# Kernel tuning notes

Hardware: AMD Instinct MI355X
Metric: run time of the kernel (lower is better)

## Reference

```python
import jax, jax.numpy as jnp
import numpy as np

EPS = 1e-5
DIM, QK, PDIM, SR = 256, 64, 128, 2
B, H, W = 16, 64, 64
SCALE = QK ** (-0.5)


def _conv(x, w, stride, pad, groups=1):
    return jax.lax.conv_general_dilated(
        x, w, (stride, stride), [(pad, pad), (pad, pad)], feature_group_count=groups)


def _bn(x, g, b, m, v):
    # inference-mode BatchNorm2d with running stats
    s = (g / jnp.sqrt(v + EPS))[None, :, None, None]
    return (x - m[None, :, None, None]) * s + b[None, :, None, None]


def _gn1(x, g, b):
    # GroupNorm(1, C): normalize over (C,H,W) per sample
    mu = x.mean(axis=(1, 2, 3), keepdims=True)
    var = x.var(axis=(1, 2, 3), keepdims=True)
    xh = (x - mu) / jnp.sqrt(var + EPS)
    return xh * g[None, :, None, None] + b[None, :, None, None]


def setup_inputs() -> dict:
    key = jax.random.key(0)
    ks = jax.random.split(key, 6)
    inp = {
        'x': jax.random.normal(ks[0], (B, DIM, H, W), jnp.float32),
        'gn_g': jnp.ones((DIM,), jnp.float32),
        'gn_b': jnp.zeros((DIM,), jnp.float32),
        'w_in': jax.random.normal(ks[1], (2 * QK + DIM, DIM, 3, 3), jnp.float32) * 0.05,
        'bn_in_g': jnp.ones((2 * QK + DIM,), jnp.float32),
        'bn_in_b': jnp.zeros((2 * QK + DIM,), jnp.float32),
        'bn_in_m': jnp.zeros((2 * QK + DIM,), jnp.float32),
        'bn_in_v': jnp.ones((2 * QK + DIM,), jnp.float32),
        'w_k': jax.random.normal(ks[2], (QK, 1, SR, SR), jnp.float32) * 0.05,
        'bn_k_g': jnp.ones((QK,), jnp.float32),
        'bn_k_b': jnp.zeros((QK,), jnp.float32),
        'bn_k_m': jnp.zeros((QK,), jnp.float32),
        'bn_k_v': jnp.ones((QK,), jnp.float32),
        'w_v': jax.random.normal(ks[3], (PDIM, 1, SR, SR), jnp.float32) * 0.05,
        'bn_v_g': jnp.ones((PDIM,), jnp.float32),
        'bn_v_b': jnp.zeros((PDIM,), jnp.float32),
        'bn_v_m': jnp.zeros((PDIM,), jnp.float32),
        'bn_v_v': jnp.ones((PDIM,), jnp.float32),
        'w_out': jax.random.normal(ks[4], (DIM, DIM, 1, 1), jnp.float32) * 0.05,
        'bn_out_g': jnp.ones((DIM,), jnp.float32),
        'bn_out_b': jnp.zeros((DIM,), jnp.float32),
        'bn_out_m': jnp.zeros((DIM,), jnp.float32),
        'bn_out_v': jnp.ones((DIM,), jnp.float32),
    }
    return inp


def reference(x, gn_g, gn_b, w_in, bn_in_g, bn_in_b, bn_in_m, bn_in_v,
              w_k, bn_k_g, bn_k_b, bn_k_m, bn_k_v,
              w_v, bn_v_g, bn_v_b, bn_v_m, bn_v_v,
              w_out, bn_out_g, bn_out_b, bn_out_m, bn_out_v):
    x = _gn1(x, gn_g, gn_b)
    y = _bn(_conv(x, w_in, 1, 1), bn_in_g, bn_in_b, bn_in_m, bn_in_v)
    q = y[:, :QK]
    k = y[:, QK:2 * QK]
    v = y[:, 2 * QK:2 * QK + PDIM]
    u = y[:, 2 * QK + PDIM:]
    # depthwise sr-stride convs reduce k/v spatially
    k = _bn(_conv(k, w_k, SR, 0, groups=QK), bn_k_g, bn_k_b, bn_k_m, bn_k_v)
    v = _bn(_conv(v, w_v, SR, 0, groups=PDIM), bn_v_g, bn_v_b, bn_v_m, bn_v_v)
    b, _, h, w = u.shape
    qf = q.reshape(b, QK, -1)      # [B, QK, N]
    kf = k.reshape(b, QK, -1)      # [B, QK, M]
    vf = v.reshape(b, PDIM, -1)    # [B, PDIM, M]
    attn = jnp.einsum('bcn,bcm->bnm', qf, kf) * SCALE
    attn = jax.nn.softmax(attn, axis=-1)
    o = jnp.einsum('bcm,bnm->bcn', vf, attn).reshape(b, PDIM, h, w)
    cat = jnp.concatenate([o, u], axis=1)
    out = _bn(_conv(jax.nn.relu(cat), w_out, 1, 0), bn_out_g, bn_out_b, bn_out_m, bn_out_v)
    return out
```

## Files before the change

### kernel.cpp

```cpp
#include <hip/hip_runtime.h>
#include <stdint.h>

#define EPSV 1e-5f

typedef __attribute__((ext_vector_type(8))) short short8;
typedef __attribute__((ext_vector_type(4))) float f32x4;
typedef __bf16 bf16x8 __attribute__((ext_vector_type(8)));

__device__ __forceinline__ unsigned short f2bf(float f) {
  union { float f; unsigned int u; } v; v.f = f;
  unsigned int r = (v.u + 0x7FFFu + ((v.u >> 16) & 1u)) >> 16;
  return (unsigned short)r;
}
__device__ __forceinline__ float bf2f(unsigned short h) {
  union { unsigned int u; float f; } v; v.u = ((unsigned int)h) << 16;
  return v.f;
}

__device__ __forceinline__ f32x4 mfma16(bf16x8 a, bf16x8 b, f32x4 c) {
  return __builtin_amdgcn_mfma_f32_16x16x32_bf16(a, b, c, 0, 0, 0);
}

#define GLOAD16(g, l)                                                          \
  __builtin_amdgcn_global_load_lds(                                            \
      (const __attribute__((address_space(1))) void*)(g),                      \
      (__attribute__((address_space(3))) void*)(l), 16, 0, 0)

__global__ __launch_bounds__(256) void k_gn_stats(const float* __restrict__ x,
                                                  float* __restrict__ stats) {
  int b = blockIdx.x >> 6, chunk = blockIdx.x & 63;
  const float4* xp = (const float4*)(x + ((size_t)b << 20) + (size_t)chunk * 16384);
  int t = threadIdx.x;
  float s = 0.f, q = 0.f;
#pragma unroll
  for (int i = 0; i < 16; ++i) {
    float4 v = xp[i * 256 + t];
    s += v.x + v.y + v.z + v.w;
    q += v.x * v.x + v.y * v.y + v.z * v.z + v.w * v.w;
  }
#pragma unroll
  for (int m = 1; m <= 32; m <<= 1) { s += __shfl_xor(s, m); q += __shfl_xor(q, m); }
  __shared__ float ls[8];
  int w = t >> 6, l = t & 63;
  if (l == 0) { ls[w * 2] = s; ls[w * 2 + 1] = q; }
  __syncthreads();
  if (t == 0) {
    float S = ls[0] + ls[2] + ls[4] + ls[6];
    float Q = ls[1] + ls[3] + ls[5] + ls[7];
    atomicAdd(&stats[b * 2], S);
    atomicAdd(&stats[b * 2 + 1], Q);
  }
}

__global__ __launch_bounds__(256) void k_gn_norm(const float* __restrict__ x,
                                                 const float* __restrict__ stats,
                                                 const float* __restrict__ g,
                                                 const float* __restrict__ bb,
                                                 unsigned short* __restrict__ xnp) {
  __shared__ float tile[64][65];
  int pt = blockIdx.x;
  int ct = blockIdx.y;
  int b = blockIdx.z;
  int t = threadIdx.x, tr = t >> 6, tc = t & 63;
  const float* xb = x + ((size_t)b << 20) + (size_t)(ct * 64) * 4096 + pt * 64;
#pragma unroll
  for (int i = 0; i < 16; ++i) {
    int r = i * 4 + tr;
    tile[r][tc] = xb[(size_t)r * 4096 + tc];
  }
  __syncthreads();
  float mu = stats[b * 2] * (1.f / 1048576.f);
  float var = stats[b * 2 + 1] * (1.f / 1048576.f) - mu * mu;
  float istd = rsqrtf(var + EPSV);
  float gg = g[ct * 64 + tc] * istd;
  float bv = bb[ct * 64 + tc];
  unsigned short* out = xnp + (((size_t)b * 66 + (pt + 1)) * 66 + 1) * 256 + ct * 64 + tc;
#pragma unroll
  for (int i = 0; i < 16; ++i) {
    int pcol = i * 4 + tr;
    float v = (tile[tc][pcol] - mu) * gg + bv;
    out[(size_t)pcol * 256] = f2bf(v);
  }
}

__global__ __launch_bounds__(256) void k_prep_wt(const float* __restrict__ w_in,
                                                 const float* __restrict__ bg,
                                                 const float* __restrict__ bv,
                                                 unsigned short* __restrict__ wt) {
  int idx = blockIdx.x * 256 + threadIdx.x;
  if (idx >= 9 * 384 * 256) return;
  int tap = idx / 98304;
  int rem = idx - tap * 98304;
  int co = rem >> 8, ci = rem & 255;
  float s = bg[co] * rsqrtf(bv[co] + EPSV);
  wt[idx] = f2bf(w_in[(size_t)(co * 256 + ci) * 9 + tap] * s);
}

__global__ __launch_bounds__(256) void k_prep_misc(
    const float* w_out, const float* og, const float* ob, const float* om, const float* ov,
    const float* big, const float* bib, const float* bim, const float* biv,
    const float* w_k, const float* kg, const float* kb, const float* km, const float* kvv,
    const float* w_v, const float* vg, const float* vb, const float* vm, const float* vvv,
    unsigned short* wo2, float* bias_in, float* bias_out,
    float* wkf, float* bias_k, float* wvf, float* bias_v) {
  int idx = blockIdx.x * 256 + threadIdx.x;
  if (idx < 65536) {
    int co = idx >> 8;
    float s = og[co] * rsqrtf(ov[co] + EPSV);
    wo2[idx] = f2bf(w_out[idx] * s);
    return;
  }
  idx -= 65536;
  if (idx < 384) {
    float s = big[idx] * rsqrtf(biv[idx] + EPSV);
    bias_in[idx] = bib[idx] - bim[idx] * s;
    return;
  }
  idx -= 384;
  if (idx < 256) {
    float s = og[idx] * rsqrtf(ov[idx] + EPSV);
    bias_out[idx] = ob[idx] - om[idx] * s;
    return;
  }
  idx -= 256;
  if (idx < 64) {
    float s = kg[idx] * rsqrtf(kvv[idx] + EPSV);
#pragma unroll
    for (int tp = 0; tp < 4; ++tp) wkf[idx * 4 + tp] = w_k[idx * 4 + tp] * s;
    bias_k[idx] = kb[idx] - km[idx] * s;
    return;
  }
  idx -= 64;
  if (idx < 128) {
    float s = vg[idx] * rsqrtf(vvv[idx] + EPSV);
#pragma unroll
    for (int tp = 0; tp < 4; ++tp) wvf[idx * 4 + tp] = w_v[idx * 4 + tp] * s;
    bias_v[idx] = vb[idx] - vm[idx] * s;
    return;
  }
}

__global__ __launch_bounds__(256) void k_conv3(const unsigned short* __restrict__ xnp,
                                               const unsigned short* __restrict__ wt,
                                               const float* __restrict__ bias_in,
                                               unsigned short* __restrict__ y) {
  int pt = blockIdx.x, cot = blockIdx.y, b = blockIdx.z;
  int p0 = pt * 128, co0 = cot * 128;
  __shared__ alignas(16) unsigned short As[128 * 64];
  __shared__ alignas(16) unsigned short Bs[128 * 64];
  int t = threadIdx.x, w = t >> 6, l = t & 63;
  int rr = t >> 3, c8 = (t & 7) * 8;
  int lg = l >> 4, lr = l & 15;

  int baseA[4];
#pragma unroll
  for (int i = 0; i < 4; ++i) {
    int p = p0 + i * 32 + rr;
    int yy = p >> 6, xx = p & 63;
    baseA[i] = ((b * 66 + yy) * 66 + xx) * 256 + c8;
  }
  int baseB = (co0 + rr) * 256 + c8;

  f32x4 acc[4][4];
#pragma unroll
  for (int i = 0; i < 4; ++i)
#pragma unroll
    for (int j = 0; j < 4; ++j) acc[i][j] = f32x4{0.f, 0.f, 0.f, 0.f};

  int wr = (w >> 1) * 64, wc = (w & 1) * 64;

  for (int tap = 0; tap < 9; ++tap) {
    int aoff = ((tap / 3) * 66 + (tap % 3)) * 256;
#pragma unroll 1
    for (int kc = 0; kc < 4; ++kc) {
      int ci0 = kc * 64;
      __syncthreads();
#pragma unroll
      for (int i = 0; i < 4; ++i) {
        GLOAD16(xnp + baseA[i] + aoff + ci0, &As[(i * 32 + w * 8) * 64]);
        GLOAD16(wt + baseB + tap * 98304 + i * 8192 + ci0, &Bs[(i * 32 + w * 8) * 64]);
      }
      __syncthreads();
      bf16x8 af[4][2], bf[4][2];
#pragma unroll
      for (int mt = 0; mt < 4; ++mt)
#pragma unroll
        for (int k2 = 0; k2 < 2; ++k2) {
          af[mt][k2] = *(const bf16x8*)&As[(wr + mt * 16 + lr) * 64 + k2 * 32 + lg * 8];
          bf[mt][k2] = *(const bf16x8*)&Bs[(wc + mt * 16 + lr) * 64 + k2 * 32 + lg * 8];
        }
#pragma unroll
      for (int mt = 0; mt < 4; ++mt)
#pragma unroll
        for (int nt = 0; nt < 4; ++nt) {
          acc[mt][nt] = mfma16(af[mt][0], bf[nt][0], acc[mt][nt]);
          acc[mt][nt] = mfma16(af[mt][1], bf[nt][1], acc[mt][nt]);
        }
    }
  }
  float bias[4];
  int coBase = co0 + wc;
#pragma unroll
  for (int nt = 0; nt < 4; ++nt) bias[nt] = bias_in[coBase + nt * 16 + lr];
#pragma unroll
  for (int mt = 0; mt < 4; ++mt) {
    int p = p0 + wr + mt * 16 + lg * 4;
#pragma unroll
    for (int r = 0; r < 4; ++r) {
      size_t rowoff = ((size_t)(b * 4096 + p + r)) * 384;
#pragma unroll
      for (int nt = 0; nt < 4; ++nt) {
        int co = coBase + nt * 16 + lr;
        float v = acc[mt][nt][r] + bias[nt];
        if (co >= 256) v = fmaxf(v, 0.f);
        y[rowoff + co] = f2bf(v);
      }
    }
  }
}

__global__ __launch_bounds__(256) void k_kv(const unsigned short* __restrict__ y,
                                            const float* __restrict__ wkf, const float* __restrict__ bias_k,
                                            const float* __restrict__ wvf, const float* __restrict__ bias_v,
                                            unsigned short* __restrict__ kk, unsigned short* __restrict__ vv) {
  int idx = blockIdx.x * 256 + threadIdx.x;
  if (idx < 16 * 1024 * 64) {
    int c = idx & 63, m = (idx >> 6) & 1023, b = idx >> 16;
    int my = m >> 5, mx = m & 31;
    float acc = bias_k[c];
#pragma unroll
    for (int tp = 0; tp < 4; ++tp) {
      int dy = tp >> 1, dx = tp & 1;
      int p = (2 * my + dy) * 64 + 2 * mx + dx;
      acc += bf2f(y[((size_t)(b * 4096 + p)) * 384 + 64 + c]) * wkf[c * 4 + tp];
    }
    kk[idx] = f2bf(acc);
  } else {
    int i2 = idx - 16 * 1024 * 64;
    if (i2 >= 16 * 128 * 1024) return;
    int m = i2 & 1023, cv = (i2 >> 10) & 127, b = i2 >> 17;
    int my = m >> 5, mx = m & 31;
    float acc = bias_v[cv];
#pragma unroll
    for (int tp = 0; tp < 4; ++tp) {
      int dy = tp >> 1, dx = tp & 1;
      int p = (2 * my + dy) * 64 + 2 * mx + dx;
      acc += bf2f(y[((size_t)(b * 4096 + p)) * 384 + 128 + cv]) * wvf[cv * 4 + tp];
    }
    vv[i2] = f2bf(acc);
  }
}

__global__ __launch_bounds__(256) void k_attn(unsigned short* __restrict__ y,
                                              const unsigned short* __restrict__ kk,
                                              const unsigned short* __restrict__ vvb) {
  int blk = blockIdx.x;
  int b = blk >> 5, ntile = blk & 31;
  int t = threadIdx.x, w = t >> 6, l = t & 63;
  int nq0 = ntile * 128 + w * 32;
  int lg = l >> 4, lr = l & 15;
  __shared__ alignas(16) unsigned short P[4][2][16][64];
  const float SC = 0.125f * 1.44269504f;

  bf16x8 qf[2][2];
#pragma unroll
  for (int qt = 0; qt < 2; ++qt)
#pragma unroll
    for (int c = 0; c < 2; ++c)
      qf[qt][c] = *(const bf16x8*)&y[((size_t)(b * 4096 + nq0 + qt * 16 + lr)) * 384 + c * 32 + lg * 8];

  f32x4 oa[2][8];
#pragma unroll
  for (int qt = 0; qt < 2; ++qt)
#pragma unroll
    for (int tt = 0; tt < 8; ++tt) oa[qt][tt] = f32x4{0.f, 0.f, 0.f, 0.f};
  float mi[2][4], li[2][4];
#pragma unroll
  for (int qt = 0; qt < 2; ++qt)
#pragma unroll
    for (int r = 0; r < 4; ++r) { mi[qt][r] = -1e30f; li[qt][r] = 0.f; }

  for (int m0 = 0; m0 < 1024; m0 += 64) {
    bf16x8 kf[4][2];
#pragma unroll
    for (int mt = 0; mt < 4; ++mt)
#pragma unroll
      for (int c = 0; c < 2; ++c)
        kf[mt][c] = *(const bf16x8*)&kk[((size_t)(b * 1024 + m0 + mt * 16 + lr)) * 64 + c * 32 + lg * 8];

#pragma unroll
    for (int qt = 0; qt < 2; ++qt) {
      f32x4 s[4];
#pragma unroll
      for (int mt = 0; mt < 4; ++mt) {
        f32x4 z = f32x4{0.f, 0.f, 0.f, 0.f};
        z = mfma16(qf[qt][0], kf[mt][0], z);
        z = mfma16(qf[qt][1], kf[mt][1], z);
        s[mt] = z;
      }
#pragma unroll
      for (int mt = 0; mt < 4; ++mt)
#pragma unroll
        for (int r = 0; r < 4; ++r) s[mt][r] *= SC;
      float rm[4];
#pragma unroll
      for (int r = 0; r < 4; ++r)
        rm[r] = fmaxf(fmaxf(s[0][r], s[1][r]), fmaxf(s[2][r], s[3][r]));
#pragma unroll
      for (int msk = 1; msk <= 8; msk <<= 1)
#pragma unroll
        for (int r = 0; r < 4; ++r) rm[r] = fmaxf(rm[r], __shfl_xor(rm[r], msk));
      float corr[4], rs[4];
#pragma unroll
      for (int r = 0; r < 4; ++r) {
        float nm = fmaxf(mi[qt][r], rm[r]);
        corr[r] = exp2f(mi[qt][r] - nm);
        mi[qt][r] = nm;
#pragma unroll
        for (int mt = 0; mt < 4; ++mt) s[mt][r] = exp2f(s[mt][r] - nm);
        rs[r] = s[0][r] + s[1][r] + s[2][r] + s[3][r];
      }
#pragma unroll
      for (int msk = 1; msk <= 8; msk <<= 1)
#pragma unroll
        for (int r = 0; r < 4; ++r) rs[r] += __shfl_xor(rs[r], msk);
#pragma unroll
      for (int r = 0; r < 4; ++r) li[qt][r] = li[qt][r] * corr[r] + rs[r];
#pragma unroll
      for (int tt = 0; tt < 8; ++tt)
#pragma unroll
        for (int r = 0; r < 4; ++r) oa[qt][tt][r] *= corr[r];
#pragma unroll
      for (int mt = 0; mt < 4; ++mt)
#pragma unroll
        for (int r = 0; r < 4; ++r)
          P[w][qt][lg * 4 + r][mt * 16 + lr] = f2bf(s[mt][r]);
    }
    __builtin_amdgcn_wave_barrier();
    bf16x8 pf[2][2];
#pragma unroll
    for (int qt = 0; qt < 2; ++qt)
#pragma unroll
      for (int mc = 0; mc < 2; ++mc)
        pf[qt][mc] = *(const bf16x8*)&P[w][qt][lr][mc * 32 + lg * 8];
#pragma unroll
    for (int tt = 0; tt < 8; ++tt) {
      bf16x8 vf0 = *(const bf16x8*)&vvb[((size_t)(b * 128 + tt * 16 + lr)) * 1024 + m0 + lg * 8];
      bf16x8 vf1 = *(const bf16x8*)&vvb[((size_t)(b * 128 + tt * 16 + lr)) * 1024 + m0 + 32 + lg * 8];
#pragma unroll
      for (int qt = 0; qt < 2; ++qt) {
        oa[qt][tt] = mfma16(pf[qt][0], vf0, oa[qt][tt]);
        oa[qt][tt] = mfma16(pf[qt][1], vf1, oa[qt][tt]);
      }
    }
  }
#pragma unroll
  for (int qt = 0; qt < 2; ++qt)
#pragma unroll
    for (int r = 0; r < 4; ++r) {
      float inv = 1.f / li[qt][r];
      int p = nq0 + qt * 16 + lg * 4 + r;
#pragma unroll
      for (int tt = 0; tt < 8; ++tt) {
        float v = oa[qt][tt][r] * inv;
        v = fmaxf(v, 0.f);
        y[((size_t)(b * 4096 + p)) * 384 + 128 + tt * 16 + lr] = f2bf(v);
      }
    }
}

__global__ __launch_bounds__(256) void k_conv1(const unsigned short* __restrict__ y,
                                               const unsigned short* __restrict__ wo2,
                                               const float* __restrict__ bias_out,
                                               float* __restrict__ out) {
  int ptile = blockIdx.x, cot = blockIdx.y, b = blockIdx.z;
  int p0 = ptile * 128, co0 = cot * 128;
  __shared__ alignas(16) unsigned short As[128 * 64];
  __shared__ alignas(16) unsigned short Bs[128 * 64];
  int t = threadIdx.x, w = t >> 6, l = t & 63;
  int rr = t >> 3, c8 = (t & 7) * 8;
  int lg = l >> 4, lr = l & 15;
  int baseA = (co0 + rr) * 256 + c8;
  size_t baseB = ((size_t)(b * 4096 + p0 + rr)) * 384 + 128 + c8;
  f32x4 acc[4][4];
#pragma unroll
  for (int i = 0; i < 4; ++i)
#pragma unroll
    for (int j = 0; j < 4; ++j) acc[i][j] = f32x4{0.f, 0.f, 0.f, 0.f};
  int wr = (w >> 1) * 64, wc = (w & 1) * 64;
#pragma unroll 1
  for (int kc = 0; kc < 4; ++kc) {
    int ci0 = kc * 64;
    __syncthreads();
#pragma unroll
    for (int i = 0; i < 4; ++i) {
      GLOAD16(wo2 + baseA + i * 8192 + ci0, &As[(i * 32 + w * 8) * 64]);
      GLOAD16(y + baseB + (size_t)i * 32 * 384 + ci0, &Bs[(i * 32 + w * 8) * 64]);
    }
    __syncthreads();
    bf16x8 af[4][2], bf[4][2];
#pragma unroll
    for (int mt = 0; mt < 4; ++mt)
#pragma unroll
      for (int k2 = 0; k2 < 2; ++k2) {
        af[mt][k2] = *(const bf16x8*)&As[(wr + mt * 16 + lr) * 64 + k2 * 32 + lg * 8];
        bf[mt][k2] = *(const bf16x8*)&Bs[(wc + mt * 16 + lr) * 64 + k2 * 32 + lg * 8];
      }
#pragma unroll
    for (int mt = 0; mt < 4; ++mt)
#pragma unroll
      for (int nt = 0; nt < 4; ++nt) {
        acc[mt][nt] = mfma16(af[mt][0], bf[nt][0], acc[mt][nt]);
        acc[mt][nt] = mfma16(af[mt][1], bf[nt][1], acc[mt][nt]);
      }
  }
#pragma unroll
  for (int mt = 0; mt < 4; ++mt)
#pragma unroll
    for (int r = 0; r < 4; ++r) {
      int co = co0 + wr + mt * 16 + lg * 4 + r;
      float bv = bias_out[co];
      size_t obase = ((size_t)(b * 256 + co)) << 12;
#pragma unroll
      for (int nt = 0; nt < 4; ++nt) {
        int p = p0 + wc + nt * 16 + lr;
        out[obase + p] = acc[mt][nt][r] + bv;
      }
    }
}

static constexpr size_t pad256(size_t x) { return (x + 255) & ~(size_t)255; }

extern "C" void kernel_launch(void* const* d_in, const int* in_sizes, int n_in,
                              void* d_out, int out_size, void* d_ws, size_t ws_size,
                              hipStream_t stream) {
  const float* x      = (const float*)d_in[0];
  const float* gn_g   = (const float*)d_in[1];
  const float* gn_b   = (const float*)d_in[2];
  const float* w_in   = (const float*)d_in[3];
  const float* bin_g  = (const float*)d_in[4];
  const float* bin_b  = (const float*)d_in[5];
  const float* bin_m  = (const float*)d_in[6];
  const float* bin_v  = (const float*)d_in[7];
  const float* w_k    = (const float*)d_in[8];
  const float* bk_g   = (const float*)d_in[9];
  const float* bk_b   = (const float*)d_in[10];
  const float* bk_m   = (const float*)d_in[11];
  const float* bk_v   = (const float*)d_in[12];
  const float* w_v    = (const float*)d_in[13];
  const float* bv_g   = (const float*)d_in[14];
  const float* bv_b   = (const float*)d_in[15];
  const float* bv_m   = (const float*)d_in[16];
  const float* bv_v   = (const float*)d_in[17];
  const float* w_out  = (const float*)d_in[18];
  const float* bo_g   = (const float*)d_in[19];
  const float* bo_b   = (const float*)d_in[20];
  const float* bo_m   = (const float*)d_in[21];
  const float* bo_v   = (const float*)d_in[22];
  float* out = (float*)d_out;

  char* ws = (char*)d_ws;
  size_t off = 0;
  float*          stats   = (float*)(ws + off);          off += pad256(128);
  unsigned short* wt      = (unsigned short*)(ws + off); off += pad256((size_t)9 * 384 * 256 * 2);
  float*          bias_in = (float*)(ws + off);          off += pad256(384 * 4);
  unsigned short* wo2     = (unsigned short*)(ws + off); off += pad256(256 * 256 * 2);
  float*          bias_out= (float*)(ws + off);          off += pad256(256 * 4);
  float*          wkf     = (float*)(ws + off);          off += pad256(64 * 4 * 4);
  float*          bias_k  = (float*)(ws + off);          off += pad256(64 * 4);
  float*          wvf     = (float*)(ws + off);          off += pad256(128 * 4 * 4);
  float*          bias_v  = (float*)(ws + off);          off += pad256(128 * 4);
  unsigned short* xnp     = (unsigned short*)(ws + off); off += pad256((size_t)16 * 66 * 66 * 256 * 2);
  unsigned short* y       = (unsigned short*)(ws + off); off += pad256((size_t)16 * 4096 * 384 * 2);
  unsigned short* kk      = (unsigned short*)(ws + off); off += pad256((size_t)16 * 1024 * 64 * 2);
  unsigned short* vv      = (unsigned short*)(ws + off); off += pad256((size_t)16 * 128 * 1024 * 2);
  (void)ws_size; (void)out_size; (void)n_in; (void)in_sizes;

  hipMemsetAsync(stats, 0, 256, stream);
  hipMemsetAsync(xnp, 0, (size_t)16 * 66 * 66 * 256 * 2, stream);

  k_gn_stats<<<1024, 256, 0, stream>>>(x, stats);
  k_prep_wt<<<3456, 256, 0, stream>>>(w_in, bin_g, bin_v, wt);
  k_prep_misc<<<260, 256, 0, stream>>>(w_out, bo_g, bo_b, bo_m, bo_v,
                                       bin_g, bin_b, bin_m, bin_v,
                                       w_k, bk_g, bk_b, bk_m, bk_v,
                                       w_v, bv_g, bv_b, bv_m, bv_v,
                                       wo2, bias_in, bias_out, wkf, bias_k, wvf, bias_v);
  k_gn_norm<<<dim3(64, 4, 16), 256, 0, stream>>>(x, stats, gn_g, gn_b, xnp);
  k_conv3<<<dim3(32, 3, 16), 256, 0, stream>>>(xnp, wt, bias_in, y);
  k_kv<<<12288, 256, 0, stream>>>(y, wkf, bias_k, wvf, bias_v, kk, vv);
  k_attn<<<512, 256, 0, stream>>>(y, kk, vv);
  k_conv1<<<dim3(32, 2, 16), 256, 0, stream>>>(y, wo2, bias_out, out);
}
```

Before: 492.9 us.

## Stage k/v reduction through LDS; lazy softmax rescale and MFMA row sums

```diff
diff --git a/kernel.cpp b/kernel.cpp
--- a/kernel.cpp
+++ b/kernel.cpp
@@ -223,31 +223,65 @@
                                             const float* __restrict__ wkf, const float* __restrict__ bias_k,
                                             const float* __restrict__ wvf, const float* __restrict__ bias_v,
                                             unsigned short* __restrict__ kk, unsigned short* __restrict__ vv) {
-  int idx = blockIdx.x * 256 + threadIdx.x;
-  if (idx < 16 * 1024 * 64) {
-    int c = idx & 63, m = (idx >> 6) & 1023, b = idx >> 16;
-    int my = m >> 5, mx = m & 31;
-    float acc = bias_k[c];
-#pragma unroll
-    for (int tp = 0; tp < 4; ++tp) {
-      int dy = tp >> 1, dx = tp & 1;
-      int p = (2 * my + dy) * 64 + 2 * mx + dx;
-      acc += bf2f(y[((size_t)(b * 4096 + p)) * 384 + 64 + c]) * wkf[c * 4 + tp];
-    }
-    kk[idx] = f2bf(acc);
-  } else {
-    int i2 = idx - 16 * 1024 * 64;
-    if (i2 >= 16 * 128 * 1024) return;
-    int m = i2 & 1023, cv = (i2 >> 10) & 127, b = i2 >> 17;
-    int my = m >> 5, mx = m & 31;
-    float acc = bias_v[cv];
-#pragma unroll
-    for (int tp = 0; tp < 4; ++tp) {
-      int dy = tp >> 1, dx = tp & 1;
-      int p = (2 * my + dy) * 64 + 2 * mx + dx;
-      acc += bf2f(y[((size_t)(b * 4096 + p)) * 384 + 128 + cv]) * wvf[cv * 4 + tp];
-    }
-    vv[i2] = f2bf(acc);
+  constexpr int LDW = 200;
+  __shared__ unsigned short ty[128 * LDW];
+  __shared__ unsigned short vt[128 * 33];
+  int b = blockIdx.x >> 5, my = blockIdx.x & 31;
+  int t = threadIdx.x;
+  const unsigned short* ybase = y + ((size_t)(b * 4096 + my * 128)) * 384 + 64;
+#pragma unroll
+  for (int j = 0; j < 12; ++j) {
+    int idx = j * 256 + t;
+    int row = idx / 24, c8 = idx - row * 24;
+    bf16x8 v = *(const bf16x8*)&ybase[(size_t)row * 384 + c8 * 8];
+    *(bf16x8*)&ty[row * LDW + c8 * 8] = v;
+  }
+  __syncthreads();
+
+  {
+    int c = t & 63, wq = t >> 6;
+    float wk0 = wkf[c * 4 + 0], wk1 = wkf[c * 4 + 1];
+    float wk2 = wkf[c * 4 + 2], wk3 = wkf[c * 4 + 3];
+    float bk = bias_k[c];
+#pragma unroll
+    for (int pass = 0; pass < 8; ++pass) {
+      int mx = pass * 4 + wq;
+      int r0 = 2 * mx, r1 = 2 * mx + 1;
+      float a = bk;
+      a += bf2f(ty[r0 * LDW + c]) * wk0;
+      a += bf2f(ty[(r0 + 1) * LDW + c]) * wk1;
+      a += bf2f(ty[(64 + r0) * LDW + c]) * wk2;
+      a += bf2f(ty[(64 + r1) * LDW + c]) * wk3;
+      kk[((size_t)(b * 1024 + my * 32 + mx)) * 64 + c] = f2bf(a);
+    }
+  }
+
+  {
+    int cv = t & 127, mxh = t >> 7;
+    float wv0 = wvf[cv * 4 + 0], wv1 = wvf[cv * 4 + 1];
+    float wv2 = wvf[cv * 4 + 2], wv3 = wvf[cv * 4 + 3];
+    float bv = bias_v[cv];
+    int col = 64 + cv;
+#pragma unroll
+    for (int pass = 0; pass < 16; ++pass) {
+      int mx = pass * 2 + mxh;
+      int r0 = 2 * mx, r1 = 2 * mx + 1;
+      float a = bv;
+      a += bf2f(ty[r0 * LDW + col]) * wv0;
+      a += bf2f(ty[r1 * LDW + col]) * wv1;
+      a += bf2f(ty[(64 + r0) * LDW + col]) * wv2;
+      a += bf2f(ty[(64 + r1) * LDW + col]) * wv3;
+      vt[cv * 33 + mx] = f2bf(a);
+    }
+  }
+  __syncthreads();
+  {
+    int mx = t & 31, cvq = t >> 5;
+#pragma unroll
+    for (int i = 0; i < 16; ++i) {
+      int cv = i * 8 + cvq;
+      vv[((size_t)(b * 128 + cv)) * 1024 + my * 32 + mx] = vt[cv * 33 + mx];
+    }
   }
 }
 
@@ -262,6 +296,11 @@
   __shared__ alignas(16) unsigned short P[4][2][16][64];
   const float SC = 0.125f * 1.44269504f;
 
+  union { short8 s; bf16x8 b; } uo;
+#pragma unroll
+  for (int i = 0; i < 8; ++i) uo.s[i] = (short)0x3F80;
+  bf16x8 ones = uo.b;
+
   bf16x8 qf[2][2];
 #pragma unroll
   for (int qt = 0; qt < 2; ++qt)
@@ -298,43 +337,36 @@
         z = mfma16(qf[qt][1], kf[mt][1], z);
         s[mt] = z;
       }
+      float rm[4];
+#pragma unroll
+      for (int r = 0; r < 4; ++r) {
+        s[0][r] *= SC; s[1][r] *= SC; s[2][r] *= SC; s[3][r] *= SC;
+        rm[r] = fmaxf(fmaxf(s[0][r], s[1][r]), fmaxf(s[2][r], s[3][r]));
+      }
+#pragma unroll
+      for (int msk = 1; msk <= 8; msk <<= 1)
+#pragma unroll
+        for (int r = 0; r < 4; ++r) rm[r] = fmaxf(rm[r], __shfl_xor(rm[r], msk));
+      bool grow = (rm[0] > mi[qt][0]) | (rm[1] > mi[qt][1]) |
+                  (rm[2] > mi[qt][2]) | (rm[3] > mi[qt][3]);
+      if (__any(grow)) {
+#pragma unroll
+        for (int r = 0; r < 4; ++r) {
+          float nm = fmaxf(mi[qt][r], rm[r]);
+          float corr = exp2f(mi[qt][r] - nm);
+          mi[qt][r] = nm;
+          li[qt][r] *= corr;
+#pragma unroll
+          for (int tt = 0; tt < 8; ++tt) oa[qt][tt][r] *= corr;
+        }
+      }
 #pragma unroll
       for (int mt = 0; mt < 4; ++mt)
 #pragma unroll
-        for (int r = 0; r < 4; ++r) s[mt][r] *= SC;
-      float rm[4];
-#pragma unroll
-      for (int r = 0; r < 4; ++r)
-        rm[r] = fmaxf(fmaxf(s[0][r], s[1][r]), fmaxf(s[2][r], s[3][r]));
-#pragma unroll
-      for (int msk = 1; msk <= 8; msk <<= 1)
-#pragma unroll
-        for (int r = 0; r < 4; ++r) rm[r] = fmaxf(rm[r], __shfl_xor(rm[r], msk));
-      float corr[4], rs[4];
-#pragma unroll
-      for (int r = 0; r < 4; ++r) {
-        float nm = fmaxf(mi[qt][r], rm[r]);
-        corr[r] = exp2f(mi[qt][r] - nm);
-        mi[qt][r] = nm;
-#pragma unroll
-        for (int mt = 0; mt < 4; ++mt) s[mt][r] = exp2f(s[mt][r] - nm);
-        rs[r] = s[0][r] + s[1][r] + s[2][r] + s[3][r];
-      }
-#pragma unroll
-      for (int msk = 1; msk <= 8; msk <<= 1)
-#pragma unroll
-        for (int r = 0; r < 4; ++r) rs[r] += __shfl_xor(rs[r], msk);
-#pragma unroll
-      for (int r = 0; r < 4; ++r) li[qt][r] = li[qt][r] * corr[r] + rs[r];
-#pragma unroll
-      for (int tt = 0; tt < 8; ++tt)
-#pragma unroll
-        for (int r = 0; r < 4; ++r) oa[qt][tt][r] *= corr[r];
-#pragma unroll
-      for (int mt = 0; mt < 4; ++mt)
-#pragma unroll
-        for (int r = 0; r < 4; ++r)
-          P[w][qt][lg * 4 + r][mt * 16 + lr] = f2bf(s[mt][r]);
+        for (int r = 0; r < 4; ++r) {
+          float e = exp2f(s[mt][r] - mi[qt][r]);
+          P[w][qt][lg * 4 + r][mt * 16 + lr] = f2bf(e);
+        }
     }
     __builtin_amdgcn_wave_barrier();
     bf16x8 pf[2][2];
@@ -343,6 +375,14 @@
 #pragma unroll
       for (int mc = 0; mc < 2; ++mc)
         pf[qt][mc] = *(const bf16x8*)&P[w][qt][lr][mc * 32 + lg * 8];
+#pragma unroll
+    for (int qt = 0; qt < 2; ++qt) {
+      f32x4 zz = f32x4{0.f, 0.f, 0.f, 0.f};
+      zz = mfma16(pf[qt][0], ones, zz);
+      zz = mfma16(pf[qt][1], ones, zz);
+#pragma unroll
+      for (int r = 0; r < 4; ++r) li[qt][r] += zz[r];
+    }
 #pragma unroll
     for (int tt = 0; tt < 8; ++tt) {
       bf16x8 vf0 = *(const bf16x8*)&vvb[((size_t)(b * 128 + tt * 16 + lr)) * 1024 + m0 + lg * 8];
@@ -488,7 +528,7 @@
                                        wo2, bias_in, bias_out, wkf, bias_k, wvf, bias_v);
   k_gn_norm<<<dim3(64, 4, 16), 256, 0, stream>>>(x, stats, gn_g, gn_b, xnp);
   k_conv3<<<dim3(32, 3, 16), 256, 0, stream>>>(xnp, wt, bias_in, y);
-  k_kv<<<12288, 256, 0, stream>>>(y, wkf, bias_k, wvf, bias_v, kk, vv);
+  k_kv<<<512, 256, 0, stream>>>(y, wkf, bias_k, wvf, bias_v, kk, vv);
   k_attn<<<512, 256, 0, stream>>>(y, kk, vv);
   k_conv1<<<dim3(32, 2, 16), 256, 0, stream>>>(y, wo2, bias_out, out);
 }
```

After: 515.2 us. 4.5% more time.
